# Performance work log

Hardware: AMD Instinct MI355X
Metric: run time of the kernel (lower is better)

Reference implementation:

```python
import jax, jax.numpy as jnp
import numpy as np

B, J, O = 32, 20, 20
D, H, F, L = 256, 8, 1024, 6
S = J * O
DH = D // H
NL = L + 1  # 6 encoder blocks + final block stacked together


def setup_inputs() -> dict:
    ks = jax.random.split(jax.random.key(0), 16)
    s = 0.02
    am = jax.random.randint(ks[4], (B, J), 0, 2) == 1
    am = am.at[:, 0].set(False)  # at least one unmasked job per row (avoid all -inf softmax)
    return {
        "operations": jax.random.normal(ks[0], (B, J, O, 2), jnp.float32),
        "job_ops_mask": jax.random.normal(ks[1], (B, J, O, O), jnp.float32),
        "ops_machines_mask": jax.random.normal(ks[2], (B, S, S), jnp.float32),
        "jobs_next_op_idx": jax.random.randint(ks[3], (B, J, 1), 0, O),
        "action_mask": am,
        "qkv_w": jax.random.normal(ks[5], (NL, 3 * D, D), jnp.float32) * s,
        "qkv_b": jnp.zeros((NL, 3 * D), jnp.float32),
        "out_w": jax.random.normal(ks[6], (NL, D, D), jnp.float32) * s,
        "out_b": jnp.zeros((NL, D), jnp.float32),
        "ln1_g": jnp.ones((NL, D), jnp.float32),
        "ln1_b": jnp.zeros((NL, D), jnp.float32),
        "ln2_g": jnp.ones((NL, D), jnp.float32),
        "ln2_b": jnp.zeros((NL, D), jnp.float32),
        "ff1_w": jax.random.normal(ks[7], (NL, F, D), jnp.float32) * s,
        "ff1_b": jnp.zeros((NL, F), jnp.float32),
        "ff2_w": jax.random.normal(ks[8], (NL, D, F), jnp.float32) * s,
        "ff2_b": jnp.zeros((NL, D), jnp.float32),
        "op_emb_w": jax.random.normal(ks[9], (D, 2), jnp.float32) * s,
        "op_emb_b": jnp.zeros((D,), jnp.float32),
        "pol_w": jax.random.normal(ks[10], (1, D), jnp.float32) * s,
        "pol_b": jnp.zeros((1,), jnp.float32),
    }


def _ln(x, g, b):
    m = x.mean(-1, keepdims=True)
    v = ((x - m) ** 2).mean(-1, keepdims=True)
    return (x - m) * jax.lax.rsqrt(v + 1e-5) * g + b


def _mha(x, mask, qw, qb, ow, ob):
    N, Sq, _ = x.shape
    qkv = x @ qw.T + qb
    q, k, v = jnp.split(qkv, 3, axis=-1)
    q = q.reshape(N, Sq, H, DH).transpose(0, 2, 1, 3)
    k = k.reshape(N, Sq, H, DH).transpose(0, 2, 1, 3)
    v = v.reshape(N, Sq, H, DH).transpose(0, 2, 1, 3)
    sc = jnp.einsum("nhqd,nhkd->nhqk", q, k) / jnp.sqrt(jnp.float32(DH))
    sc = sc + mask  # additive float attn mask, broadcast over heads where needed
    a = jax.nn.softmax(sc, axis=-1)
    o = jnp.einsum("nhqk,nhkd->nhqd", a, v).transpose(0, 2, 1, 3).reshape(N, Sq, D)
    return o @ ow.T + ob


def _forward(operations, job_ops_mask, ops_machines_mask, jobs_next_op_idx, action_mask,
             qkv_w, qkv_b, out_w, out_b, ln1_g, ln1_b, ln2_g, ln2_b,
             ff1_w, ff1_b, ff2_w, ff2_b, op_emb_w, op_emb_b, pol_w, pol_b):
    def block(x, mask, i):  # pre-norm TransformerEncoderLayer, gelu, dropout=0
        h = _ln(x, ln1_g[i], ln1_b[i])
        x = x + _mha(h, mask, qkv_w[i], qkv_b[i], out_w[i], out_b[i])
        h = _ln(x, ln2_g[i], ln2_b[i])
        ff = jax.nn.gelu(h @ ff1_w[i].T + ff1_b[i], approximate=False) @ ff2_w[i].T + ff2_b[i]
        return x + ff

    # sinusoidal positional encoding over the operation index
    pos = jnp.arange(O, dtype=jnp.float32)[:, None]
    div = jnp.exp(jnp.arange(0, D, 2, dtype=jnp.float32) * (-np.log(10000.0) / D))
    pe = jnp.stack([jnp.sin(pos * div), jnp.cos(pos * div)], axis=-1).reshape(O, D)
    x = operations @ op_emb_w.T + op_emb_b + pe[None, None]  # (B,J,O,D)

    # ALiBi slopes: 1/x^(i+1), x = 256^(1/H)
    base = (2.0 ** 8) ** (1.0 / H)
    slope = (1.0 / base ** jnp.arange(1, H + 1, dtype=jnp.float32))[None, :, None, None]
    job_mask = job_ops_mask.reshape(B * J, 1, O, O) * slope  # (B*J, H, O, O)
    mach_mask = ops_machines_mask[:, None, :, :]  # (B, 1, S, S), identical across heads

    for i in range(L):
        if i % 2 == 0:  # per-job attention over operations
            x = block(x.reshape(B * J, O, D), job_mask, i).reshape(B, J, O, D)
        else:  # per-machine attention over all operations
            x = block(x.reshape(B, S, D), mach_mask, i).reshape(B, J, O, D)

    idx = jnp.broadcast_to(jobs_next_op_idx[:, :, :, None], (B, J, 1, D))
    nxt = jnp.take_along_axis(x, idx, axis=2)[:, :, 0, :]  # (B, J, D)
    kp = jnp.where(action_mask, -jnp.inf, 0.0)[:, None, None, :]  # key padding mask
    nxt = block(nxt, kp, L)
    logits = (nxt @ pol_w.T + pol_b)[:, :, 0]
    return jnp.where(action_mask, -jnp.inf, logits)


def reference(operations, job_ops_mask, ops_machines_mask, jobs_next_op_idx, action_mask,
              qkv_w, qkv_b, out_w, out_b, ln1_g, ln1_b, ln2_g, ln2_b,
              ff1_w, ff1_b, ff2_w, ff2_b, op_emb_w, op_emb_b, pol_w, pol_b):
    return _forward(operations, job_ops_mask, ops_machines_mask, jobs_next_op_idx, action_mask,
                    qkv_w, qkv_b, out_w, out_b, ln1_g, ln1_b, ln2_g, ln2_b,
                    ff1_w, ff1_b, ff2_w, ff2_b, op_emb_w, op_emb_b, pol_w, pol_b)
```

## Files before the change

### kernel.cpp

```cpp
#include <hip/hip_runtime.h>
#include <math.h>

#define B_  32
#define J_  20
#define O_  20
#define S_  400
#define D_  256
#define H_  8
#define F_  1024
#define L_  6
#define T_  12800
#define T2_ 640

#define NEG_BIG (-1e30f)

typedef __attribute__((ext_vector_type(8))) short short8;
typedef __attribute__((ext_vector_type(4))) float f32x4;

__device__ __forceinline__ short f2b(float f) {
  union { float f; unsigned u; } c; c.f = f;
  unsigned r = (c.u + 0x7FFFu + ((c.u >> 16) & 1u)) >> 16;
  return (short)r;
}
__device__ __forceinline__ float b2f(short s) {
  union { unsigned u; float f; } c;
  c.u = ((unsigned)(unsigned short)s) << 16;
  return c.f;
}
__device__ __forceinline__ unsigned addpk(unsigned a, unsigned b) {
  union { unsigned u; float f; } x, y;
  x.u = a << 16;        y.u = b << 16;        float lo = x.f + y.f;
  x.u = a & 0xffff0000u; y.u = b & 0xffff0000u; float hi = x.f + y.f;
  return (unsigned)(unsigned short)f2b(lo) | ((unsigned)(unsigned short)f2b(hi) << 16);
}
__device__ __forceinline__ void async_copy16(const short* g, short* l) {
  __builtin_amdgcn_global_load_lds(
      (const __attribute__((address_space(1))) void*)g,
      (__attribute__((address_space(3))) void*)l, 16, 0, 0);
}

__global__ __launch_bounds__(256) void k_f2b4(
    const float* __restrict__ s0, short* __restrict__ d0,
    const float* __restrict__ s1, short* __restrict__ d1,
    const float* __restrict__ s2, short* __restrict__ d2,
    const float* __restrict__ s3, short* __restrict__ d3,
    const float* __restrict__ s4, short* __restrict__ d4)
{
  int bid = blockIdx.x;
  const float* src; short* dst; int base;
  if (bid < 672)        { src = s0; dst = d0; base = bid; }
  else if (bid < 896)   { src = s1; dst = d1; base = bid - 672; }
  else if (bid < 1792)  { src = s2; dst = d2; base = bid - 896; }
  else if (bid < 2688)  { src = s3; dst = d3; base = bid - 1792; }
  else                  { src = s4; dst = d4; base = bid - 2688; }
  int i = (base * 256 + threadIdx.x) * 8;
  float4 a = *(const float4*)(src + i);
  float4 b = *(const float4*)(src + i + 4);
  short8 o;
  o[0] = f2b(a.x); o[1] = f2b(a.y); o[2] = f2b(a.z); o[3] = f2b(a.w);
  o[4] = f2b(b.x); o[5] = f2b(b.y); o[6] = f2b(b.z); o[7] = f2b(b.w);
  *(short8*)(dst + i) = o;
}

__global__ __launch_bounds__(640) void k_maskconv(
    const void* __restrict__ am_raw, int* __restrict__ am_out)
{
  __shared__ int isInt32;
  const int tid = threadIdx.x;
  if (tid == 0) isInt32 = 1;
  __syncthreads();
  if (tid < 160) {
    int v = ((const int*)am_raw)[tid];
    if (v != 0 && v != 1) atomicAnd(&isInt32, 0);
  }
  __syncthreads();
  if (tid < 640) {
    int v;
    if (isInt32) v = ((const int*)am_raw)[tid] != 0;
    else         v = ((const unsigned char*)am_raw)[tid] != 0;
    am_out[tid] = v;
  }
}

__global__ __launch_bounds__(256) void k_embed(
    const float* __restrict__ ops, const float* __restrict__ ew,
    const float* __restrict__ eb, short* __restrict__ x)
{
  int idx = blockIdx.x * 256 + threadIdx.x;
  int d = idx & 255;
  int t = idx >> 8;
  int o = t % O_;
  float a0 = ops[(size_t)t * 2 + 0], a1 = ops[(size_t)t * 2 + 1];
  int k = d >> 1;
  float div = expf((float)(2 * k) * -0.03597789207803197f);
  float ang = (float)o * div;
  float pe = (d & 1) ? cosf(ang) : sinf(ang);
  x[idx] = f2b(a0 * ew[d * 2 + 0] + a1 * ew[d * 2 + 1] + eb[d] + pe);
}

__global__ __launch_bounds__(256) void k_ln(
    const short* __restrict__ x, const float* __restrict__ g, const float* __restrict__ b,
    short* __restrict__ out, int nTok)
{
  int gid = blockIdx.x * 256 + threadIdx.x;
  int tok = gid >> 6, lane = threadIdx.x & 63;
  if (tok >= nTok) return;
  int2 pk = ((const int2*)(x + (size_t)tok * 256))[lane];
  union { unsigned u; float f; } c;
  float vx, vy, vz, vw;
  c.u = (unsigned)pk.x << 16;        vx = c.f;
  c.u = (unsigned)pk.x & 0xffff0000u; vy = c.f;
  c.u = (unsigned)pk.y << 16;        vz = c.f;
  c.u = (unsigned)pk.y & 0xffff0000u; vw = c.f;
  float s = vx + vy + vz + vw;
  #pragma unroll
  for (int off = 32; off > 0; off >>= 1) s += __shfl_down(s, off);
  float mean = __shfl(s, 0) * (1.f / 256.f);
  float dx = vx - mean, dy = vy - mean, dz = vz - mean, dw = vw - mean;
  float q = dx * dx + dy * dy + dz * dz + dw * dw;
  #pragma unroll
  for (int off = 32; off > 0; off >>= 1) q += __shfl_down(q, off);
  float var = __shfl(q, 0) * (1.f / 256.f);
  float inv = 1.f / sqrtf(var + 1e-5f);
  float4 gv = ((const float4*)g)[lane];
  float4 bv = ((const float4*)b)[lane];
  float ox = dx * inv * gv.x + bv.x;
  float oy = dy * inv * gv.y + bv.y;
  float oz = dz * inv * gv.z + bv.z;
  float ow = dw * inv * gv.w + bv.w;
  int2 po;
  po.x = (int)(unsigned short)f2b(ox) | ((int)(unsigned short)f2b(oy) << 16);
  po.y = (int)(unsigned short)f2b(oz) | ((int)(unsigned short)f2b(ow) << 16);
  ((int2*)(out + (size_t)tok * 256))[lane] = po;
}

__global__ __launch_bounds__(256) void k_gemm_bf16(
    const short* __restrict__ A, const short* __restrict__ W,
    const float* __restrict__ bias, const short* __restrict__ R,
    short* __restrict__ C, int M, int N, int K, int act)
{
  __shared__ short LDS_[17408];
  short* Asf = LDS_;
  short* Bsf = LDS_ + 8192;
  short* Csf = LDS_;
  const int tid  = threadIdx.x;
  const int lane = tid & 63;
  const int wv   = tid >> 6;
  const int lm   = lane & 15;
  const int quad = lane >> 4;
  const int wm   = (wv >> 1) * 64;
  const int wn   = (wv & 1) * 64;
  const int n0 = blockIdx.x * 128;
  const int m0 = blockIdx.y * 128;

  f32x4 acc[4][4] = {};

  for (int k0 = 0; k0 < K; k0 += 64) {
    __syncthreads();
    #pragma unroll
    for (int i = 0; i < 4; ++i) {
      const int c    = tid + 256 * i;
      const int row  = c >> 3;
      const int kc8  = ((c & 7) ^ (row & 7)) * 8;
      async_copy16(A + (size_t)(m0 + row) * K + k0 + kc8, &Asf[c * 8]);
      async_copy16(W + (size_t)(n0 + row) * K + k0 + kc8, &Bsf[c * 8]);
    }
    __syncthreads();
    #pragma unroll
    for (int kh = 0; kh < 2; ++kh) {
      short8 af[4], bf[4];
      #pragma unroll
      for (int i = 0; i < 4; ++i) {
        const int row  = wm + i * 16 + lm;
        const int slot = (kh * 4 + quad) ^ (lm & 7);
        af[i] = *(short8*)&Asf[(row * 8 + slot) * 8];
      }
      #pragma unroll
      for (int j = 0; j < 4; ++j) {
        const int row  = wn + j * 16 + lm;
        const int slot = (kh * 4 + quad) ^ (lm & 7);
        bf[j] = *(short8*)&Bsf[(row * 8 + slot) * 8];
      }
      #pragma unroll
      for (int i = 0; i < 4; ++i)
        #pragma unroll
        for (int j = 0; j < 4; ++j)
          acc[i][j] = __builtin_amdgcn_mfma_f32_16x16x32_bf16(af[i], bf[j], acc[i][j], 0, 0, 0);
    }
  }

  __syncthreads();
  #pragma unroll
  for (int j = 0; j < 4; ++j) {
    const int ccol = wn + j * 16 + lm;
    const float bv = bias[n0 + ccol];
    #pragma unroll
    for (int i = 0; i < 4; ++i) {
      #pragma unroll
      for (int r = 0; r < 4; ++r) {
        const int row = wm + i * 16 + quad * 4 + r;
        float vvv = acc[i][j][r] + bv;
        if (act) vvv = vvv / (1.f + __expf(-1.702f * vvv));
        Csf[row * 136 + ccol] = f2b(vvv);
      }
    }
  }
  __syncthreads();
  {
    const int srow = tid >> 1, sh = (tid & 1) * 64;
    const size_t gbase = (size_t)(m0 + srow) * N + n0 + sh;
    const short* ls = &Csf[srow * 136 + sh];
    #pragma unroll
    for (int u = 0; u < 8; ++u) {
      uint4 v = *(const uint4*)(ls + u * 8);
      if (R) {
        uint4 rv = *(const uint4*)(R + gbase + u * 8);
        v.x = addpk(v.x, rv.x); v.y = addpk(v.y, rv.y);
        v.z = addpk(v.z, rv.z); v.w = addpk(v.w, rv.w);
      }
      *(uint4*)(C + gbase + u * 8) = v;
    }
  }
}

__global__ __launch_bounds__(256) void k_gemm_ln(
    const short* __restrict__ A, const short* __restrict__ W,
    const float* __restrict__ bias, const short* __restrict__ R,
    short* __restrict__ X, short* __restrict__ Hout,
    const float* __restrict__ g, const float* __restrict__ bb_,
    int M, int K)
{
  __shared__ short LDS_[4096 + 16896];
  short* Asf = LDS_;
  short* Bsf = LDS_ + 4096;
  short* Csf = LDS_ + 4096;
  const int tid  = threadIdx.x;
  const int lane = tid & 63;
  const int wv   = tid >> 6;
  const int lm   = lane & 15;
  const int quad = lane >> 4;
  const int wn   = wv * 64;
  const int m0   = blockIdx.x * 64;

  f32x4 acc[4][4] = {};

  for (int k0 = 0; k0 < K; k0 += 64) {
    __syncthreads();
    #pragma unroll
    for (int i = 0; i < 2; ++i) {
      const int c   = tid + 256 * i;
      const int row = c >> 3;
      const int kc8 = ((c & 7) ^ (row & 7)) * 8;
      async_copy16(A + (size_t)(m0 + row) * K + k0 + kc8, &Asf[c * 8]);
    }
    #pragma unroll
    for (int i = 0; i < 8; ++i) {
      const int c   = tid + 256 * i;
      const int row = c >> 3;
      const int kc8 = ((c & 7) ^ (row & 7)) * 8;
      async_copy16(W + (size_t)row * K + k0 + kc8, &Bsf[c * 8]);
    }
    __syncthreads();
    #pragma unroll
    for (int kh = 0; kh < 2; ++kh) {
      short8 af[4], bf[4];
      #pragma unroll
      for (int i = 0; i < 4; ++i) {
        const int row  = i * 16 + lm;
        const int slot = (kh * 4 + quad) ^ (lm & 7);
        af[i] = *(short8*)&Asf[(row * 8 + slot) * 8];
      }
      #pragma unroll
      for (int j = 0; j < 4; ++j) {
        const int row  = wn + j * 16 + lm;
        const int slot = (kh * 4 + quad) ^ (lm & 7);
        bf[j] = *(short8*)&Bsf[(row * 8 + slot) * 8];
      }
      #pragma unroll
      for (int i = 0; i < 4; ++i)
        #pragma unroll
        for (int j = 0; j < 4; ++j)
          acc[i][j] = __builtin_amdgcn_mfma_f32_16x16x32_bf16(af[i], bf[j], acc[i][j], 0, 0, 0);
    }
  }

  __syncthreads();
  #pragma unroll
  for (int j = 0; j < 4; ++j) {
    const int ccol = wn + j * 16 + lm;
    const float bv = bias[ccol];
    #pragma unroll
    for (int i = 0; i < 4; ++i) {
      #pragma unroll
      for (int r = 0; r < 4; ++r) {
        const int row = i * 16 + quad * 4 + r;
        Csf[row * 264 + ccol] = f2b(acc[i][j][r] + bv);
      }
    }
  }
  __syncthreads();

  {
    const int row = tid >> 2, cb = (tid & 3) * 64;
    const size_t gbase = (size_t)(m0 + row) * 256 + cb;
    const short* ls = &Csf[row * 264 + cb];
    uint4 xv[8];
    float s1 = 0.f, s2 = 0.f;
    #pragma unroll
    for (int u = 0; u < 8; ++u) {
      uint4 v = *(const uint4*)(ls + u * 8);
      uint4 rv = *(const uint4*)(R + gbase + u * 8);
      v.x = addpk(v.x, rv.x); v.y = addpk(v.y, rv.y);
      v.z = addpk(v.z, rv.z); v.w = addpk(v.w, rv.w);
      xv[u] = v;
      *(uint4*)(X + gbase + u * 8) = v;
      #pragma unroll
      for (int w2 = 0; w2 < 4; ++w2) {
        unsigned pv = (&v.x)[w2];
        union { unsigned u; float f; } c1, c2;
        c1.u = pv << 16; c2.u = pv & 0xffff0000u;
        s1 += c1.f + c2.f;
        s2 += c1.f * c1.f + c2.f * c2.f;
      }
    }
    s1 += __shfl_xor(s1, 1); s2 += __shfl_xor(s2, 1);
    s1 += __shfl_xor(s1, 2); s2 += __shfl_xor(s2, 2);
    const float mean = s1 * (1.f / 256.f);
    const float var  = s2 * (1.f / 256.f) - mean * mean;
    const float inv  = 1.f / sqrtf(var + 1e-5f);
    #pragma unroll
    for (int u = 0; u < 8; ++u) {
      float4 g0 = *(const float4*)(g + cb + u * 8);
      float4 g1 = *(const float4*)(g + cb + u * 8 + 4);
      float4 b0 = *(const float4*)(bb_ + cb + u * 8);
      float4 b1 = *(const float4*)(bb_ + cb + u * 8 + 4);
      auto lnpk = [&](unsigned pv, float ga, float gb2, float ba, float bb2) -> unsigned {
        union { unsigned u; float f; } c1, c2;
        c1.u = pv << 16; c2.u = pv & 0xffff0000u;
        float lo = (c1.f - mean) * inv * ga + ba;
        float hi = (c2.f - mean) * inv * gb2 + bb2;
        return (unsigned)(unsigned short)f2b(lo) | ((unsigned)(unsigned short)f2b(hi) << 16);
      };
      uint4 hv;
      hv.x = lnpk(xv[u].x, g0.x, g0.y, b0.x, b0.y);
      hv.y = lnpk(xv[u].y, g0.z, g0.w, b0.z, b0.w);
      hv.z = lnpk(xv[u].z, g1.x, g1.y, b1.x, b1.y);
      hv.w = lnpk(xv[u].w, g1.z, g1.w, b1.z, b1.w);
      *(uint4*)(Hout + gbase + u * 8) = hv;
    }
  }
}

#define QSTR 776
#define PSTR20 40
__global__ __launch_bounds__(512) void k_attn20_mfma(
    const short* __restrict__ qkv, short* __restrict__ att,
    const float* __restrict__ jmask, const int* __restrict__ amask, int mode)
{
  __shared__ short QK[32 * QSTR];
  __shared__ short Ps[8][32 * PSTR20];
  const int seq  = blockIdx.x;
  const int tid  = threadIdx.x;
  const int wv   = tid >> 6;
  const int lane = tid & 63;
  const int l15  = lane & 15;
  const int quad = lane >> 4;
  const float scale = 0.1767766952966369f;

  for (int e = tid; e < 3072; e += 512) {
    int row = e / 96, c8 = (e % 96) * 8;
    uint4 v = {0u, 0u, 0u, 0u};
    if (row < 20) v = *(const uint4*)(qkv + ((size_t)seq * 20 + row) * 768 + c8);
    *(uint4*)&QK[row * QSTR + c8] = v;
  }
  __syncthreads();

  const short8 aq0 = *(short8*)&QK[(0  + l15) * QSTR + wv * 32 + quad * 8];
  const short8 aq1 = *(short8*)&QK[(16 + l15) * QSTR + wv * 32 + quad * 8];
  const short8 bk0 = *(short8*)&QK[(0  + l15) * QSTR + 256 + wv * 32 + quad * 8];
  const short8 bk1 = *(short8*)&QK[(16 + l15) * QSTR + 256 + wv * 32 + quad * 8];
  f32x4 z4 = {0.f, 0.f, 0.f, 0.f};
  f32x4 s00 = __builtin_amdgcn_mfma_f32_16x16x32_bf16(aq0, bk0, z4, 0, 0, 0);
  f32x4 s01 = __builtin_amdgcn_mfma_f32_16x16x32_bf16(aq0, bk1, z4, 0, 0, 0);
  f32x4 s10 = __builtin_amdgcn_mfma_f32_16x16x32_bf16(aq1, bk0, z4, 0, 0, 0);
  f32x4 s11 = __builtin_amdgcn_mfma_f32_16x16x32_bf16(aq1, bk1, z4, 0, 0, 0);

  const float slope = exp2f(-(float)(wv + 1));
  short* psw = &Ps[wv][0];
  float l0[4] = {0.f, 0.f, 0.f, 0.f};
  float l1[4] = {0.f, 0.f, 0.f, 0.f};

  #pragma unroll
  for (int kt = 0; kt < 2; ++kt) {
    const int k  = kt * 16 + l15;
    const int kc = (k < 20) ? k : 19;
    float madd1 = 0.f;
    if (mode == 1) madd1 = amask[seq * 20 + kc] ? NEG_BIG : 0.f;
    #pragma unroll
    for (int qt = 0; qt < 2; ++qt) {
      f32x4 s = (kt == 0) ? (qt == 0 ? s00 : s10) : (qt == 0 ? s01 : s11);
      #pragma unroll
      for (int r = 0; r < 4; ++r) {
        const int q  = qt * 16 + quad * 4 + r;
        const int qc = (q < 20) ? q : 19;
        float sv = s[r] * scale;
        if (mode == 0) sv += jmask[(size_t)seq * 400 + qc * 20 + kc] * slope;
        else           sv += madd1;
        float p = (k < 20) ? __expf(fminf(sv, 40.f)) : 0.f;
        if (qt == 0) l0[r] += p; else l1[r] += p;
        psw[q * PSTR20 + k] = f2b(p);
      }
    }
  }
  #pragma unroll
  for (int r = 0; r < 4; ++r) {
    float t0 = l0[r];
    t0 += __shfl_xor(t0, 1); t0 += __shfl_xor(t0, 2);
    t0 += __shfl_xor(t0, 4); t0 += __shfl_xor(t0, 8);
    l0[r] = 1.f / t0;
    float t1 = l1[r];
    t1 += __shfl_xor(t1, 1); t1 += __shfl_xor(t1, 2);
    t1 += __shfl_xor(t1, 4); t1 += __shfl_xor(t1, 8);
    l1[r] = 1.f / t1;
  }

  const short8 pf0 = *(short8*)&psw[(0  + l15) * PSTR20 + quad * 8];
  const short8 pf1 = *(short8*)&psw[(16 + l15) * PSTR20 + quad * 8];
  #pragma unroll
  for (int dt = 0; dt < 2; ++dt) {
    const int d = wv * 32 + dt * 16 + l15;
    short8 vf;
    #pragma unroll
    for (int j = 0; j < 8; ++j)
      vf[j] = QK[(quad * 8 + j) * QSTR + 512 + d];
    f32x4 o0 = __builtin_amdgcn_mfma_f32_16x16x32_bf16(pf0, vf, z4, 0, 0, 0);
    f32x4 o1 = __builtin_amdgcn_mfma_f32_16x16x32_bf16(pf1, vf, z4, 0, 0, 0);
    #pragma unroll
    for (int r = 0; r < 4; ++r) {
      const int q = quad * 4 + r;
      att[((size_t)seq * 20 + q) * 256 + d] = f2b(o0[r] * l0[r]);
    }
    if (quad == 0) {
      #pragma unroll
      for (int r = 0; r < 4; ++r) {
        const int q = 16 + r;
        att[((size_t)seq * 20 + q) * 256 + d] = f2b(o1[r] * l1[r]);
      }
    }
  }
}

#define VSTR 36
#define PSTRW 40
#define MSTR 424
__global__ __launch_bounds__(512) void k_attn400_mfma(
    const short* __restrict__ qkv, short* __restrict__ att,
    const short* __restrict__ mbf)
{
  __shared__ short Wl[8 * 1792];
  __shared__ short Ml[16 * MSTR];

  const int id   = blockIdx.x;
  const int b    = (id >> 3) / 25 * 8 + (id & 7);
  const int qt   = (id >> 3) % 25;
  const int tid  = threadIdx.x;
  const int wv   = tid >> 6;
  const int lane = tid & 63;
  const int l15  = lane & 15;
  const int quad = lane >> 4;
  const int q0   = qt * 16;
  const float scale = 0.1767766952966369f;

  for (int e = tid; e < 16 * 52; e += 512) {
    const int row = e / 52, cc = e % 52;
    uint4 v = {0u, 0u, 0u, 0u};
    if (cc < 50)
      v = *(const uint4*)(mbf + ((size_t)(b * 400 + q0 + row)) * 400 + cc * 8);
    *(uint4*)&Ml[row * MSTR + cc * 8] = v;
  }

  short* Vw = &Wl[wv * 1792];
  short* Pw = &Wl[wv * 1792 + 1152];
  const short* qbase = qkv + (size_t)b * 400 * 768;

  const short8 af = *(const short8*)(qbase + (size_t)(q0 + l15) * 768 + wv * 32 + quad * 8);

  f32x4 accO[2] = {};
  float lsum = 0.f;

  const int vrow = lane >> 1;
  const int vch  = (lane & 1) * 2;
  const int vdst = vrow * VSTR + vch * 8;

  short8 kf0, kf1;
  uint4  nv0, nv1;
  auto prefK = [&](int k0) {
    kf0 = *(const short8*)(qbase + (size_t)(k0 + l15) * 768 + 256 + wv * 32 + quad * 8);
    int kr = k0 + 16 + l15; if (kr > 399) kr = 399;
    kf1 = *(const short8*)(qbase + (size_t)kr * 768 + 256 + wv * 32 + quad * 8);
  };
  auto prefV = [&](int k0) {
    int vr = k0 + vrow; if (vr > 399) vr = 399;
    const short* vp = qbase + (size_t)vr * 768 + 512 + wv * 32 + vch * 8;
    nv0 = *(const uint4*)vp;
    nv1 = *(const uint4*)(vp + 8);
  };
  prefK(0);
  prefV(0);

  __syncthreads();

  const short* mrow = &Ml[l15 * MSTR];

  for (int k0 = 0; k0 < 416; k0 += 32) {
    const uint4 v0 = nv0, v1 = nv1;
    const short8 ck0 = kf0, ck1 = kf1;

    *(uint4*)&Vw[vdst]     = v0;
    *(uint4*)&Vw[vdst + 8] = v1;

    f32x4 z4 = {0.f, 0.f, 0.f, 0.f};
    f32x4 s0 = __builtin_amdgcn_mfma_f32_16x16x32_bf16(ck0, af, z4, 0, 0, 0);
    f32x4 s1 = __builtin_amdgcn_mfma_f32_16x16x32_bf16(ck1, af, z4, 0, 0, 0);

    if (k0 + 32 < 416) { prefK(k0 + 32); prefV(k0 + 32); }

    uint2 ma = *(const uint2*)(mrow + k0 + quad * 4);
    uint2 mb = *(const uint2*)(mrow + k0 + 16 + quad * 4);
    float mAv[4], mBv[4];
    {
      union { unsigned u; float f; } c;
      c.u = ma.x << 16;         mAv[0] = c.f;
      c.u = ma.x & 0xffff0000u; mAv[1] = c.f;
      c.u = ma.y << 16;         mAv[2] = c.f;
      c.u = ma.y & 0xffff0000u; mAv[3] = c.f;
      c.u = mb.x << 16;         mBv[0] = c.f;
      c.u = mb.x & 0xffff0000u; mBv[1] = c.f;
      c.u = mb.y << 16;         mBv[2] = c.f;
      c.u = mb.y & 0xffff0000u; mBv[3] = c.f;
    }

    float p0[4], p1[4];
    #pragma unroll
    for (int r = 0; r < 4; ++r) {
      const int kB = k0 + 16 + quad * 4 + r;
      float svA = s0[r] * scale + mAv[r];
      float svB = (kB < 400) ? (s1[r] * scale + mBv[r]) : NEG_BIG;
      p0[r] = __expf(fminf(svA, 40.f));
      p1[r] = __expf(fminf(svB, 40.f));
      lsum += p0[r] + p1[r];
    }

    unsigned pk00, pk01, pk10, pk11;
    asm("v_cvt_pk_bf16_f32 %0, %1, %2" : "=v"(pk00) : "v"(p0[0]), "v"(p0[1]));
    asm("v_cvt_pk_bf16_f32 %0, %1, %2" : "=v"(pk01) : "v"(p0[2]), "v"(p0[3]));
    asm("v_cvt_pk_bf16_f32 %0, %1, %2" : "=v"(pk10) : "v"(p1[0]), "v"(p1[1]));
    asm("v_cvt_pk_bf16_f32 %0, %1, %2" : "=v"(pk11) : "v"(p1[2]), "v"(p1[3]));
    uint2 w0; w0.x = pk00; w0.y = pk01;
    uint2 w1; w1.x = pk10; w1.y = pk11;
    *(uint2*)&Pw[l15 * PSTRW + quad * 4]      = w0;
    *(uint2*)&Pw[l15 * PSTRW + 16 + quad * 4] = w1;
    const short8 pf = *(short8*)&Pw[l15 * PSTRW + quad * 8];

    #pragma unroll
    for (int c = 0; c < 2; ++c) {
      short8 vf;
      #pragma unroll
      for (int j = 0; j < 8; ++j)
        vf[j] = Vw[(quad * 8 + j) * VSTR + c * 16 + l15];
      accO[c] = __builtin_amdgcn_mfma_f32_16x16x32_bf16(vf, pf, accO[c], 0, 0, 0);
    }
  }

  lsum += __shfl_xor(lsum, 16);
  lsum += __shfl_xor(lsum, 32);
  const float inv = 1.f / lsum;

  #pragma unroll
  for (int c = 0; c < 2; ++c) {
    float a0 = accO[c][0] * inv, a1 = accO[c][1] * inv;
    float a2 = accO[c][2] * inv, a3 = accO[c][3] * inv;
    unsigned o01, o23;
    asm("v_cvt_pk_bf16_f32 %0, %1, %2" : "=v"(o01) : "v"(a0), "v"(a1));
    asm("v_cvt_pk_bf16_f32 %0, %1, %2" : "=v"(o23) : "v"(a2), "v"(a3));
    uint2 ov; ov.x = o01; ov.y = o23;
    *(uint2*)&att[((size_t)b * 400 + q0 + l15) * 256 + wv * 32 + c * 16 + quad * 4] = ov;
  }
}

__global__ __launch_bounds__(256) void k_gather2(
    const short* __restrict__ x, const short* __restrict__ h,
    const int* __restrict__ idx, short* __restrict__ x2, short* __restrict__ h2)
{
  int t = blockIdx.x * 256 + threadIdx.x;
  if (t >= 640 * 16) return;
  int bj = t >> 4, c = t & 15;
  int o = idx[bj];
  size_t src = ((size_t)bj * 20 + o) * 256;
  ((uint4*)(x2 + (size_t)bj * 256))[c] = ((const uint4*)(x + src))[c];
  ((uint4*)(h2 + (size_t)bj * 256))[c] = ((const uint4*)(h + src))[c];
}

__global__ __launch_bounds__(256) void k_logits(
    const short* __restrict__ x2, const float* __restrict__ pw, const float* __restrict__ pb,
    const int* __restrict__ am, float* __restrict__ out)
{
  int gid = blockIdx.x * 256 + threadIdx.x;
  int row = gid >> 6, lane = threadIdx.x & 63;
  int2 pk = ((const int2*)(x2 + (size_t)row * 256))[lane];
  union { unsigned u; float f; } c;
  float vx, vy, vz, vw;
  c.u = (unsigned)pk.x << 16;         vx = c.f;
  c.u = (unsigned)pk.x & 0xffff0000u; vy = c.f;
  c.u = (unsigned)pk.y << 16;         vz = c.f;
  c.u = (unsigned)pk.y & 0xffff0000u; vw = c.f;
  float4 w = ((const float4*)pw)[lane];
  float s = vx * w.x + vy * w.y + vz * w.z + vw * w.w;
  #pragma unroll
  for (int off = 32; off > 0; off >>= 1) s += __shfl_down(s, off);
  if (lane == 0) out[row] = am[row] ? NEG_BIG : (s + pb[0]);
}

extern "C" void kernel_launch(void* const* d_in, const int* in_sizes, int n_in,
                              void* d_out, int out_size, void* d_ws, size_t ws_size,
                              hipStream_t stream)
{
  (void)in_sizes; (void)n_in; (void)out_size; (void)ws_size;
  const float* operations        = (const float*)d_in[0];
  const float* job_ops_mask      = (const float*)d_in[1];
  const float* ops_machines_mask = (const float*)d_in[2];
  const int*   jobs_next_op_idx  = (const int*)d_in[3];
  const void*  action_mask_raw   = (const void*)d_in[4];
  const float* qkv_w = (const float*)d_in[5];
  const float* qkv_b = (const float*)d_in[6];
  const float* out_w = (const float*)d_in[7];
  const float* out_b = (const float*)d_in[8];
  const float* ln1_g = (const float*)d_in[9];
  const float* ln1_b = (const float*)d_in[10];
  const float* ln2_g = (const float*)d_in[11];
  const float* ln2_b = (const float*)d_in[12];
  const float* ff1_w = (const float*)d_in[13];
  const float* ff1_b = (const float*)d_in[14];
  const float* ff2_w = (const float*)d_in[15];
  const float* ff2_b = (const float*)d_in[16];
  const float* op_emb_w = (const float*)d_in[17];
  const float* op_emb_b = (const float*)d_in[18];
  const float* pol_w = (const float*)d_in[19];
  const float* pol_b = (const float*)d_in[20];
  float* out = (float*)d_out;

  short* x    = (short*)d_ws;
  short* x2   = x + (size_t)T_ * D_;
  short* h    = x2 + (size_t)T2_ * D_;
  short* big  = h + (size_t)T_ * D_;
  short* h2   = big + (size_t)T_ * F_;
  short* big2 = h2 + (size_t)T2_ * D_;
  int*   amc  = (int*)(big2 + (size_t)T2_ * F_);
  short* bwq  = (short*)(amc + 640);
  short* bwo  = bwq + (size_t)7 * 768 * 256;
  short* bwf1 = bwo + (size_t)7 * 256 * 256;
  short* bwf2 = bwf1 + (size_t)7 * 1024 * 256;
  short* mbf  = bwf2 + (size_t)7 * 256 * 1024;

  auto gemm = [&](const short* A, const short* Wb, const float* bias, const short* R,
                  short* C, int M, int N, int K, int act) {
    k_gemm_bf16<<<dim3(N / 128, M / 128), dim3(256), 0, stream>>>(
        A, Wb, bias, R, C, M, N, K, act);
  };
  auto gemm_ln = [&](const short* A, const short* Wb, const float* bias, const short* R,
                     short* X, short* Hout, const float* g, const float* b, int M, int K) {
    k_gemm_ln<<<dim3(M / 64), dim3(256), 0, stream>>>(
        A, Wb, bias, R, X, Hout, g, b, M, K);
  };

  k_f2b4<<<dim3(5188), 256, 0, stream>>>(qkv_w, bwq, out_w, bwo, ff1_w, bwf1,
                                         ff2_w, bwf2, ops_machines_mask, mbf);
  k_maskconv<<<dim3(1), dim3(640), 0, stream>>>(action_mask_raw, amc);
  k_embed<<<dim3(T_ * D_ / 256), dim3(256), 0, stream>>>(operations, op_emb_w, op_emb_b, x);
  k_ln<<<dim3(T_ / 4), 256, 0, stream>>>(x, ln1_g, ln1_b, h, T_);

  for (int i = 0; i < L_; ++i) {
    const short* qw  = bwq  + (size_t)i * 768 * 256;
    const float* qb  = qkv_b + (size_t)i * 768;
    const short* ow  = bwo  + (size_t)i * 256 * 256;
    const float* ob  = out_b + (size_t)i * 256;
    const short* f1w = bwf1 + (size_t)i * 1024 * 256;
    const float* f1b = ff1_b + (size_t)i * 1024;
    const short* f2w = bwf2 + (size_t)i * 256 * 1024;
    const float* f2b_ = ff2_b + (size_t)i * 256;
    gemm(h, qw, qb, nullptr, big, T_, 768, 256, 0);
    if ((i & 1) == 0)
      k_attn20_mfma<<<dim3(640), 512, 0, stream>>>(big, h, job_ops_mask, nullptr, 0);
    else
      k_attn400_mfma<<<dim3(800), 512, 0, stream>>>(big, h, mbf);
    gemm_ln(h, ow, ob, x, x, h, ln2_g + i * D_, ln2_b + i * D_, T_, 256);
    gemm(h, f1w, f1b, nullptr, big, T_, 1024, 256, 1);
    gemm_ln(big, f2w, f2b_, x, x, h, ln1_g + (i + 1) * D_, ln1_b + (i + 1) * D_, T_, 1024);
  }

  k_gather2<<<dim3(40), 256, 0, stream>>>(x, h, jobs_next_op_idx, x2, h2);

  {
    int i = L_;
    const short* qw  = bwq  + (size_t)i * 768 * 256;
    const float* qb  = qkv_b + (size_t)i * 768;
    const short* ow  = bwo  + (size_t)i * 256 * 256;
    const float* ob  = out_b + (size_t)i * 256;
    const short* f1w = bwf1 + (size_t)i * 1024 * 256;
    const float* f1b = ff1_b + (size_t)i * 1024;
    const short* f2w = bwf2 + (size_t)i * 256 * 1024;
    const float* f2b_ = ff2_b + (size_t)i * 256;
    gemm(h2, qw, qb, nullptr, big2, T2_, 768, 256, 0);
    k_attn20_mfma<<<dim3(32), 512, 0, stream>>>(big2, h2, nullptr, amc, 1);
    gemm_ln(h2, ow, ob, x2, x2, h2, ln2_g + i * D_, ln2_b + i * D_, T2_, 256);
    gemm(h2, f1w, f1b, nullptr, big2, T2_, 1024, 256, 1);
    gemm(big2, f2w, f2b_, x2, x2, T2_, 256, 1024, 0);
  }

  k_logits<<<dim3(160), 256, 0, stream>>>(x2, pol_w, pol_b, amc, out);
}
```

Before: 974.1 us.

## Pre-transpose V into a separate buffer for the 400-token attention

```diff
diff --git a/kernel.cpp b/kernel.cpp
--- a/kernel.cpp
+++ b/kernel.cpp
@@ -450,14 +450,47 @@
   }
 }
 
-#define VSTR 36
+#define VTS 416
+__global__ __launch_bounds__(256) void k_vtrans(
+    const short* __restrict__ qkv, short* __restrict__ vt)
+{
+  __shared__ short T[64][73];
+  const int bid = blockIdx.x;
+  const int b  = bid / 28, rem = bid % 28;
+  const int kt = rem / 4, dt = rem % 4;
+  const int k0 = kt * 64, d0 = dt * 64;
+  const int tid = threadIdx.x;
+  #pragma unroll
+  for (int i = 0; i < 2; ++i) {
+    const int c = tid + 256 * i;
+    const int row = c >> 3, cc = (c & 7) * 8;
+    const int tok = k0 + row;
+    uint4 v = {0u, 0u, 0u, 0u};
+    if (tok < 400)
+      v = *(const uint4*)(qkv + ((size_t)(b * 400 + tok)) * 768 + 512 + d0 + cc);
+    *(uint4*)&T[row][cc] = v;
+  }
+  __syncthreads();
+  #pragma unroll
+  for (int i = 0; i < 2; ++i) {
+    const int c = tid + 256 * i;
+    const int dl = c >> 3, kk = (c & 7) * 8;
+    if (k0 + kk < VTS) {
+      short8 o;
+      #pragma unroll
+      for (int j = 0; j < 8; ++j) o[j] = T[kk + j][dl];
+      *(short8*)(vt + ((size_t)(b * 256 + d0 + dl)) * VTS + k0 + kk) = o;
+    }
+  }
+}
+
 #define PSTRW 40
 #define MSTR 424
 __global__ __launch_bounds__(512) void k_attn400_mfma(
-    const short* __restrict__ qkv, short* __restrict__ att,
-    const short* __restrict__ mbf)
-{
-  __shared__ short Wl[8 * 1792];
+    const short* __restrict__ qkv, const short* __restrict__ vt,
+    short* __restrict__ att, const short* __restrict__ mbf)
+{
+  __shared__ short Pl[8][16 * PSTRW];
   __shared__ short Ml[16 * MSTR];
 
   const int id   = blockIdx.x;
@@ -479,31 +512,24 @@
     *(uint4*)&Ml[row * MSTR + cc * 8] = v;
   }
 
-  short* Vw = &Wl[wv * 1792];
-  short* Pw = &Wl[wv * 1792 + 1152];
+  short* Pw = &Pl[wv][0];
   const short* qbase = qkv + (size_t)b * 400 * 768;
+  const short* vtb   = vt + ((size_t)b * 256 + wv * 32) * VTS;
 
   const short8 af = *(const short8*)(qbase + (size_t)(q0 + l15) * 768 + wv * 32 + quad * 8);
 
   f32x4 accO[2] = {};
   float lsum = 0.f;
 
-  const int vrow = lane >> 1;
-  const int vch  = (lane & 1) * 2;
-  const int vdst = vrow * VSTR + vch * 8;
-
-  short8 kf0, kf1;
-  uint4  nv0, nv1;
+  short8 kf0, kf1, nvf0, nvf1;
   auto prefK = [&](int k0) {
     kf0 = *(const short8*)(qbase + (size_t)(k0 + l15) * 768 + 256 + wv * 32 + quad * 8);
     int kr = k0 + 16 + l15; if (kr > 399) kr = 399;
     kf1 = *(const short8*)(qbase + (size_t)kr * 768 + 256 + wv * 32 + quad * 8);
   };
   auto prefV = [&](int k0) {
-    int vr = k0 + vrow; if (vr > 399) vr = 399;
-    const short* vp = qbase + (size_t)vr * 768 + 512 + wv * 32 + vch * 8;
-    nv0 = *(const uint4*)vp;
-    nv1 = *(const uint4*)(vp + 8);
+    nvf0 = *(const short8*)(vtb + (size_t)(0  + l15) * VTS + k0 + quad * 8);
+    nvf1 = *(const short8*)(vtb + (size_t)(16 + l15) * VTS + k0 + quad * 8);
   };
   prefK(0);
   prefV(0);
@@ -513,11 +539,8 @@
   const short* mrow = &Ml[l15 * MSTR];
 
   for (int k0 = 0; k0 < 416; k0 += 32) {
-    const uint4 v0 = nv0, v1 = nv1;
     const short8 ck0 = kf0, ck1 = kf1;
-
-    *(uint4*)&Vw[vdst]     = v0;
-    *(uint4*)&Vw[vdst + 8] = v1;
+    const short8 cv0 = nvf0, cv1 = nvf1;
 
     f32x4 z4 = {0.f, 0.f, 0.f, 0.f};
     f32x4 s0 = __builtin_amdgcn_mfma_f32_16x16x32_bf16(ck0, af, z4, 0, 0, 0);
@@ -562,14 +585,8 @@
     *(uint2*)&Pw[l15 * PSTRW + 16 + quad * 4] = w1;
     const short8 pf = *(short8*)&Pw[l15 * PSTRW + quad * 8];
 
-    #pragma unroll
-    for (int c = 0; c < 2; ++c) {
-      short8 vf;
-      #pragma unroll
-      for (int j = 0; j < 8; ++j)
-        vf[j] = Vw[(quad * 8 + j) * VSTR + c * 16 + l15];
-      accO[c] = __builtin_amdgcn_mfma_f32_16x16x32_bf16(vf, pf, accO[c], 0, 0, 0);
-    }
+    accO[0] = __builtin_amdgcn_mfma_f32_16x16x32_bf16(cv0, pf, accO[0], 0, 0, 0);
+    accO[1] = __builtin_amdgcn_mfma_f32_16x16x32_bf16(cv1, pf, accO[1], 0, 0, 0);
   }
 
   lsum += __shfl_xor(lsum, 16);
@@ -661,6 +678,7 @@
   short* bwf1 = bwo + (size_t)7 * 256 * 256;
   short* bwf2 = bwf1 + (size_t)7 * 1024 * 256;
   short* mbf  = bwf2 + (size_t)7 * 256 * 1024;
+  short* vt   = mbf + (size_t)B_ * 400 * 400;
 
   auto gemm = [&](const short* A, const short* Wb, const float* bias, const short* R,
                   short* C, int M, int N, int K, int act) {
@@ -689,10 +707,12 @@
     const short* f2w = bwf2 + (size_t)i * 256 * 1024;
     const float* f2b_ = ff2_b + (size_t)i * 256;
     gemm(h, qw, qb, nullptr, big, T_, 768, 256, 0);
-    if ((i & 1) == 0)
+    if ((i & 1) == 0) {
       k_attn20_mfma<<<dim3(640), 512, 0, stream>>>(big, h, job_ops_mask, nullptr, 0);
-    else
-      k_attn400_mfma<<<dim3(800), 512, 0, stream>>>(big, h, mbf);
+    } else {
+      k_vtrans<<<dim3(896), 256, 0, stream>>>(big, vt);
+      k_attn400_mfma<<<dim3(800), 512, 0, stream>>>(big, vt, h, mbf);
+    }
     gemm_ln(h, ow, ob, x, x, h, ln2_g + i * D_, ln2_b + i * D_, T_, 256);
     gemm(h, f1w, f1b, nullptr, big, T_, 1024, 256, 1);
     gemm_ln(big, f2w, f2b_, x, x, h, ln1_g + (i + 1) * D_, ln1_b + (i + 1) * D_, T_, 1024);
```

Result: no change. 961.0 us (-1.3%).
